# Kernel tuning notes

Measured on AMD Instinct MI355X. Metric: run time of the kernel, lower is better.

The kernel has to match this reference:

```python
import jax, jax.numpy as jnp
import numpy as np

N_PAIRS = 64000
N_ATOMS = 16000
N_PAIR_FEATURES = 8
N_HIDDEN = 100


def setup_inputs() -> dict:
    key = jax.random.key(0)
    k1, k2, k3, k4 = jax.random.split(key, 4)
    pair_features = jax.random.normal(k1, (N_PAIRS, N_PAIR_FEATURES), dtype=jnp.float32)
    atom_features = jax.random.normal(k2, (N_ATOMS, N_HIDDEN), dtype=jnp.float32)
    atom_to_pair = jax.random.randint(k3, (N_PAIRS, 2), 0, N_ATOMS, dtype=jnp.int32)
    W = jax.random.normal(k4, (N_PAIR_FEATURES, N_HIDDEN * N_HIDDEN), dtype=jnp.float32) * 0.1
    b = jnp.zeros((N_HIDDEN * N_HIDDEN,), dtype=jnp.float32)
    return {"pair_features": pair_features, "atom_features": atom_features,
            "atom_to_pair": atom_to_pair, "W": W, "b": b}


def reference(pair_features, atom_features, atom_to_pair, W, b):
    n_atoms, n_hidden = atom_features.shape
    # Dense projection: [E, F] @ [F, H*H] -> per-edge HxH matrices
    A = (pair_features @ W + b).reshape(-1, n_hidden, n_hidden)  # [E, H, H]
    # Gather source-atom features (column 1 of atom_to_pair)
    src = atom_features[atom_to_pair[:, 1]]                      # [E, H]
    # Batched matrix-vector multiply per edge
    msg = jnp.einsum('eij,ej->ei', A, src)                       # [E, H]
    # Scatter-reduce messages onto destination atoms (column 0)
    return jax.ops.segment_sum(msg, atom_to_pair[:, 0], num_segments=n_atoms)
```

## Files before the change

### kernel.cpp

```cpp
#include <hip/hip_runtime.h>
#include <hip/hip_bf16.h>

#define N_PAIRS   64000
#define N_ATOMS   16000
#define N_FEAT    8
#define N_HIDDEN  100
#define SW        1024
#define SKL       936
#define MAX_DEG   32

#define SETUP_BLOCKS (112 * 1024 / 256)
#define HIST_BLOCKS  (N_PAIRS / 256)

typedef __attribute__((ext_vector_type(8))) short bf16x8_t;
typedef __attribute__((ext_vector_type(4))) float f32x4_t;

__global__ __launch_bounds__(256) void zero_wtb2(const float* __restrict__ W,
                                                 const float* __restrict__ b,
                                                 __hip_bfloat16* __restrict__ wtb2,
                                                 int* __restrict__ deg) {
    int id = blockIdx.x * 256 + threadIdx.x;
    if (id < N_ATOMS) deg[id] = 0;
    int i = id >> 10;
    int k = id & 1023;
    float v = 0.f;
    if (i < N_HIDDEN) {
        if (k < 800) {
            int f = k / N_HIDDEN;
            int j = k - f * N_HIDDEN;
            v = W[f * (N_HIDDEN * N_HIDDEN) + i * N_HIDDEN + j];
        } else if (k < 900) {
            v = b[i * N_HIDDEN + (k - 800)];
        }
    }
    wtb2[id] = __float2bfloat16(v);
}

__global__ __launch_bounds__(256) void hist(const int* __restrict__ a2p,
                                            int* __restrict__ deg,
                                            unsigned* __restrict__ bucket) {
    int e = blockIdx.x * 256 + threadIdx.x;
    int dest = a2p[e * 2];
    int src  = a2p[e * 2 + 1];
    int slot = atomicAdd(&deg[dest], 1);
    if (slot < MAX_DEG)
        bucket[dest * MAX_DEG + slot] = ((unsigned)e << 14) | (unsigned)src;
}

__global__ __launch_bounds__(512) void fused_edge_gemm(const float* __restrict__ af,
                                                       const float* __restrict__ pf,
                                                       const int* __restrict__ deg,
                                                       const unsigned* __restrict__ bucket,
                                                       const __hip_bfloat16* __restrict__ wtb2,
                                                       float* __restrict__ out) {
    __shared__ __hip_bfloat16 St[16 * SKL];
    int blk  = blockIdx.x;
    int wave = threadIdx.x >> 6;
    int lane = threadIdx.x & 63;
    bool act = (lane < 50);

#pragma unroll
    for (int j = 0; j < 2; ++j) {
        int r = wave * 2 + j;
        int d = __builtin_amdgcn_readfirstlane(blk * 16 + r);
        int n = deg[d];
        if (n > MAX_DEG) n = MAX_DEG;

        const unsigned* sb = bucket + (size_t)d * MAX_DEG;

        float acc[9][2] = {};
        for (int t0 = 0; t0 < n; t0 += 4) {
            float2 a[4];
            unsigned pk[4];
#pragma unroll
            for (int u = 0; u < 4; ++u) {
                int t = t0 + u;
                pk[u] = sb[t < n ? t : 0];
                int src = (int)(pk[u] & 16383u);
                if (t < n && act)
                    a[u] = *(const float2*)(af + src * N_HIDDEN + 2 * lane);
                else
                    a[u] = make_float2(0.f, 0.f);
            }
#pragma unroll
            for (int u = 0; u < 4; ++u) {
                int e = (int)(pk[u] >> 14);
                const float* pe = pf + e * N_FEAT;
#pragma unroll
                for (int f = 0; f < N_FEAT; ++f) {
                    float p = pe[f];
                    acc[f][0] += p * a[u].x;
                    acc[f][1] += p * a[u].y;
                }
                acc[8][0] += a[u].x;
                acc[8][1] += a[u].y;
            }
        }

        __hip_bfloat16* srow = St + r * SKL;
        if (act) {
#pragma unroll
            for (int f = 0; f < 9; ++f) {
                __hip_bfloat162 h;
                h.x = __float2bfloat16(acc[f][0]);
                h.y = __float2bfloat16(acc[f][1]);
                *(__hip_bfloat162*)(srow + f * N_HIDDEN + 2 * lane) = h;
            }
        } else {
            __hip_bfloat162 z;
            z.x = __float2bfloat16(0.f);
            z.y = z.x;
            *(__hip_bfloat162*)(srow + 900 + 2 * (lane - 50)) = z;
        }
    }
    __syncthreads();

    if (wave < 7) {
        int quad = lane >> 4;
        int l15  = lane & 15;
        int m0   = blk * 16;
        const __hip_bfloat16* as = St + l15 * SKL + quad * 8;
        const __hip_bfloat16* bp = wtb2 + (size_t)(wave * 16 + l15) * SW + quad * 8;
        f32x4_t accd = {0.f, 0.f, 0.f, 0.f};
#pragma unroll
        for (int k = 0; k < 29; ++k) {
            bf16x8_t aa = *(const bf16x8_t*)(as + k * 32);
            bf16x8_t bb = *(const bf16x8_t*)(bp + k * 32);
            accd = __builtin_amdgcn_mfma_f32_16x16x32_bf16(aa, bb, accd, 0, 0, 0);
        }
        int c = wave * 16 + l15;
        if (c < N_HIDDEN) {
#pragma unroll
            for (int rr = 0; rr < 4; ++rr)
                out[(size_t)(m0 + quad * 4 + rr) * N_HIDDEN + c] = accd[rr];
        }
    }
}

extern "C" void kernel_launch(void* const* d_in, const int* in_sizes, int n_in,
                              void* d_out, int out_size, void* d_ws, size_t ws_size,
                              hipStream_t stream) {
    const float* pf  = (const float*)d_in[0];
    const float* af  = (const float*)d_in[1];
    const int*   a2p = (const int*)d_in[2];
    const float* W   = (const float*)d_in[3];
    const float* b   = (const float*)d_in[4];
    float* out = (float*)d_out;

    char* ws = (char*)d_ws;
    __hip_bfloat16* wtb2 = (__hip_bfloat16*)ws;
    int* deg             = (int*)(ws + 229376);
    unsigned* bucket     = (unsigned*)(ws + 229376 + 64000);

    zero_wtb2<<<SETUP_BLOCKS, 256, 0, stream>>>(W, b, wtb2, deg);
    hist<<<HIST_BLOCKS, 256, 0, stream>>>(a2p, deg, bucket);
    fused_edge_gemm<<<N_ATOMS / 16, 512, 0, stream>>>(af, pf, deg, bucket, wtb2, out);
}
```

Baseline: 104.3 us.

## Double atoms per block, split MFMA K across waves, merge hist with weight prep

The fused kernel now handles 32 destination atoms per 1024-thread block instead of 16. Each weight fragment loaded from global memory feeds two MFMAs (two 16-row tiles), and the K loop is split between two wave groups whose partial sums are combined through shared memory. The W/b bf16 repacking moves out of the zeroing kernel into the histogram kernel as extra blocks, so it runs alongside the atomic binning. The larger blocks and extra LDS reduce occupancy and add a barrier in exchange for halving weight traffic per atom.

```diff
diff --git a/kernel.cpp b/kernel.cpp
--- a/kernel.cpp
+++ b/kernel.cpp
@@ -9,51 +9,58 @@
 #define SKL       936
 #define MAX_DEG   32
 
-#define SETUP_BLOCKS (112 * 1024 / 256)
+#define ZERO_BLOCKS  ((N_ATOMS + 255) / 256)
 #define HIST_BLOCKS  (N_PAIRS / 256)
+#define WTB2_BLOCKS  (112 * 1024 / 256)
+#define D2_BLOCKS    (HIST_BLOCKS + WTB2_BLOCKS)
 
 typedef __attribute__((ext_vector_type(8))) short bf16x8_t;
 typedef __attribute__((ext_vector_type(4))) float f32x4_t;
 
-__global__ __launch_bounds__(256) void zero_wtb2(const float* __restrict__ W,
-                                                 const float* __restrict__ b,
-                                                 __hip_bfloat16* __restrict__ wtb2,
-                                                 int* __restrict__ deg) {
+__global__ __launch_bounds__(256) void zero_deg(int* __restrict__ deg) {
     int id = blockIdx.x * 256 + threadIdx.x;
     if (id < N_ATOMS) deg[id] = 0;
-    int i = id >> 10;
-    int k = id & 1023;
-    float v = 0.f;
-    if (i < N_HIDDEN) {
-        if (k < 800) {
-            int f = k / N_HIDDEN;
-            int j = k - f * N_HIDDEN;
-            v = W[f * (N_HIDDEN * N_HIDDEN) + i * N_HIDDEN + j];
-        } else if (k < 900) {
-            v = b[i * N_HIDDEN + (k - 800)];
-        }
-    }
-    wtb2[id] = __float2bfloat16(v);
 }
 
-__global__ __launch_bounds__(256) void hist(const int* __restrict__ a2p,
-                                            int* __restrict__ deg,
-                                            unsigned* __restrict__ bucket) {
-    int e = blockIdx.x * 256 + threadIdx.x;
-    int dest = a2p[e * 2];
-    int src  = a2p[e * 2 + 1];
-    int slot = atomicAdd(&deg[dest], 1);
-    if (slot < MAX_DEG)
-        bucket[dest * MAX_DEG + slot] = ((unsigned)e << 14) | (unsigned)src;
+__global__ __launch_bounds__(256) void hist_wtb2(const int* __restrict__ a2p,
+                                                 const float* __restrict__ W,
+                                                 const float* __restrict__ b,
+                                                 int* __restrict__ deg,
+                                                 unsigned* __restrict__ bucket,
+                                                 __hip_bfloat16* __restrict__ wtb2) {
+    int bid = blockIdx.x;
+    if (bid < HIST_BLOCKS) {
+        int e = bid * 256 + threadIdx.x;
+        int2 pr = ((const int2*)a2p)[e];
+        int slot = atomicAdd(&deg[pr.x], 1);
+        if (slot < MAX_DEG)
+            bucket[pr.x * MAX_DEG + slot] = ((unsigned)e << 14) | (unsigned)pr.y;
+    } else {
+        int id = (bid - HIST_BLOCKS) * 256 + threadIdx.x;
+        int i = id >> 10;
+        int k = id & 1023;
+        float v = 0.f;
+        if (i < N_HIDDEN) {
+            if (k < 800) {
+                int f = k / N_HIDDEN;
+                int j = k - f * N_HIDDEN;
+                v = W[f * (N_HIDDEN * N_HIDDEN) + i * N_HIDDEN + j];
+            } else if (k < 900) {
+                v = b[i * N_HIDDEN + (k - 800)];
+            }
+        }
+        wtb2[id] = __float2bfloat16(v);
+    }
 }
 
-__global__ __launch_bounds__(512) void fused_edge_gemm(const float* __restrict__ af,
-                                                       const float* __restrict__ pf,
-                                                       const int* __restrict__ deg,
-                                                       const unsigned* __restrict__ bucket,
-                                                       const __hip_bfloat16* __restrict__ wtb2,
-                                                       float* __restrict__ out) {
-    __shared__ __hip_bfloat16 St[16 * SKL];
+__global__ __launch_bounds__(1024) void fused_edge_gemm(const float* __restrict__ af,
+                                                        const float* __restrict__ pf,
+                                                        const int* __restrict__ deg,
+                                                        const unsigned* __restrict__ bucket,
+                                                        const __hip_bfloat16* __restrict__ wtb2,
+                                                        float* __restrict__ out) {
+    __shared__ __hip_bfloat16 St[32 * SKL];
+    __shared__ float Pb[14 * 256];
     int blk  = blockIdx.x;
     int wave = threadIdx.x >> 6;
     int lane = threadIdx.x & 63;
@@ -62,7 +69,7 @@
 #pragma unroll
     for (int j = 0; j < 2; ++j) {
         int r = wave * 2 + j;
-        int d = __builtin_amdgcn_readfirstlane(blk * 16 + r);
+        int d = __builtin_amdgcn_readfirstlane(blk * 32 + r);
         int n = deg[d];
         if (n > MAX_DEG) n = MAX_DEG;
 
@@ -115,24 +122,46 @@
     }
     __syncthreads();
 
+    int quad = lane >> 4;
+    int l15  = lane & 15;
+    int wt   = (wave < 7) ? wave : ((wave >= 8 && wave < 15) ? wave - 8 : -1);
+    f32x4_t acc0 = {0.f, 0.f, 0.f, 0.f};
+    f32x4_t acc1 = {0.f, 0.f, 0.f, 0.f};
+    if (wt >= 0) {
+        int kb = (wave < 7) ? 0 : 14;
+        int ke = (wave < 7) ? 14 : 29;
+        const __hip_bfloat16* as0 = St + l15 * SKL + quad * 8;
+        const __hip_bfloat16* as1 = St + (16 + l15) * SKL + quad * 8;
+        const __hip_bfloat16* bp  = wtb2 + (size_t)(wt * 16 + l15) * SW + quad * 8;
+        for (int k = kb; k < ke; ++k) {
+            bf16x8_t bb = *(const bf16x8_t*)(bp + k * 32);
+            bf16x8_t a0 = *(const bf16x8_t*)(as0 + k * 32);
+            bf16x8_t a1 = *(const bf16x8_t*)(as1 + k * 32);
+            acc0 = __builtin_amdgcn_mfma_f32_16x16x32_bf16(a0, bb, acc0, 0, 0, 0);
+            acc1 = __builtin_amdgcn_mfma_f32_16x16x32_bf16(a1, bb, acc1, 0, 0, 0);
+        }
+        if (wave >= 8) {
+            float* p0 = Pb + (wt * 2 + 0) * 256 + quad * 4 * 16 + l15;
+            float* p1 = Pb + (wt * 2 + 1) * 256 + quad * 4 * 16 + l15;
+#pragma unroll
+            for (int rr = 0; rr < 4; ++rr) {
+                p0[rr * 16] = acc0[rr];
+                p1[rr * 16] = acc1[rr];
+            }
+        }
+    }
+    __syncthreads();
+
     if (wave < 7) {
-        int quad = lane >> 4;
-        int l15  = lane & 15;
-        int m0   = blk * 16;
-        const __hip_bfloat16* as = St + l15 * SKL + quad * 8;
-        const __hip_bfloat16* bp = wtb2 + (size_t)(wave * 16 + l15) * SW + quad * 8;
-        f32x4_t accd = {0.f, 0.f, 0.f, 0.f};
-#pragma unroll
-        for (int k = 0; k < 29; ++k) {
-            bf16x8_t aa = *(const bf16x8_t*)(as + k * 32);
-            bf16x8_t bb = *(const bf16x8_t*)(bp + k * 32);
-            accd = __builtin_amdgcn_mfma_f32_16x16x32_bf16(aa, bb, accd, 0, 0, 0);
-        }
         int c = wave * 16 + l15;
         if (c < N_HIDDEN) {
+            const float* p0 = Pb + (wave * 2 + 0) * 256 + quad * 4 * 16 + l15;
+            const float* p1 = Pb + (wave * 2 + 1) * 256 + quad * 4 * 16 + l15;
 #pragma unroll
-            for (int rr = 0; rr < 4; ++rr)
-                out[(size_t)(m0 + quad * 4 + rr) * N_HIDDEN + c] = accd[rr];
+            for (int rr = 0; rr < 4; ++rr) {
+                out[(size_t)(blk * 32 + quad * 4 + rr) * N_HIDDEN + c] = acc0[rr] + p0[rr * 16];
+                out[(size_t)(blk * 32 + 16 + quad * 4 + rr) * N_HIDDEN + c] = acc1[rr] + p1[rr * 16];
+            }
         }
     }
 }
@@ -152,7 +181,7 @@
     int* deg             = (int*)(ws + 229376);
     unsigned* bucket     = (unsigned*)(ws + 229376 + 64000);
 
-    zero_wtb2<<<SETUP_BLOCKS, 256, 0, stream>>>(W, b, wtb2, deg);
-    hist<<<HIST_BLOCKS, 256, 0, stream>>>(a2p, deg, bucket);
-    fused_edge_gemm<<<N_ATOMS / 16, 512, 0, stream>>>(af, pf, deg, bucket, wtb2, out);
+    zero_deg<<<ZERO_BLOCKS, 256, 0, stream>>>(deg);
+    hist_wtb2<<<D2_BLOCKS, 256, 0, stream>>>(a2p, W, b, deg, bucket, wtb2);
+    fused_edge_gemm<<<N_ATOMS / 32, 1024, 0, stream>>>(af, pf, deg, bucket, wtb2, out);
 }
```

Measured after the change: 92.67 us. 1.13x faster.
